# Performance work log

Hardware: AMD Instinct MI355X
Metric: run time of the kernel (lower is better)

## Reference

```python
import jax, jax.numpy as jnp
import numpy as np

N_NODES = 100000
N_EDGES = 1600000
IN_CH = 128
NHIDDEN = 64
OUT_CH = 40
NLAYERS = 4
ALPHA = 0.1


def setup_inputs() -> dict:
    key = jax.random.key(0)
    ks = jax.random.split(key, 7)
    x = jax.random.normal(ks[0], (N_NODES, IN_CH), dtype=jnp.float32)
    edge_index = jax.random.randint(ks[1], (2, N_EDGES), 0, N_NODES, dtype=jnp.int64)
    batch_graph = jnp.zeros((N_NODES,), dtype=jnp.int64)
    fc1_w = jax.random.normal(ks[2], (NHIDDEN, IN_CH), dtype=jnp.float32) * (1.0 / np.sqrt(IN_CH))
    fc1_b = jax.random.normal(ks[3], (NHIDDEN,), dtype=jnp.float32) * 0.01
    conv_w = jax.random.normal(ks[4], (NLAYERS, NHIDDEN, NHIDDEN), dtype=jnp.float32) * (1.0 / np.sqrt(NHIDDEN))
    fc2_w = jax.random.normal(ks[5], (OUT_CH, NHIDDEN), dtype=jnp.float32) * (1.0 / np.sqrt(NHIDDEN))
    fc2_b = jax.random.normal(ks[6], (OUT_CH,), dtype=jnp.float32) * 0.01
    return {"x": x, "edge_index": edge_index, "batch_graph": batch_graph,
            "fc1_w": fc1_w, "fc1_b": fc1_b, "conv_w": conv_w,
            "fc2_w": fc2_w, "fc2_b": fc2_b}


def reference(x, edge_index, batch_graph, fc1_w, fc1_b, conv_w, fc2_w, fc2_b):
    # eval mode: dropout layers are identity
    n = x.shape[0]
    row, col = edge_index[0], edge_index[1]  # source, target

    # gcn_norm with add_self_loops=False: sym deg^-1/2 normalization
    deg = jax.ops.segment_sum(jnp.ones_like(row, dtype=x.dtype), col, num_segments=n)
    dinv = jnp.where(deg > 0, deg ** -0.5, 0.0)
    norm = (dinv[row] * dinv[col])[:, None]  # [E, 1]

    h = jax.nn.relu(x @ fc1_w.T + fc1_b)  # [N, nhidden]
    h0 = h
    nlayers = conv_w.shape[0]
    for i in range(nlayers):
        # GCN2Conv: aggregate, initial-residual mix, weight1 matmul (beta=1)
        agg = jax.ops.segment_sum(h[row] * norm, col, num_segments=n)
        mixed = (1.0 - ALPHA) * agg + ALPHA * h0
        h = jax.nn.relu(mixed @ conv_w[i])
    out = h @ fc2_w.T + fc2_b  # [N, out_channels]
    return out
```

## Files before the change

### kernel.cpp

```cpp
#include <hip/hip_runtime.h>
#include <hip/hip_fp16.h>

#define N_NODES 100000
#define N_EDGES 1600000
#define IN_CH   128
#define NHID    64
#define OUT_CH  40
#define NBLK    391
#define NBUCK   196
#define BCAP    8960
#define WECAP   320
#define E4CAP   (N_EDGES + 7 * N_NODES + 64)


__global__ __launch_bounds__(256) void k_scan1(const int* __restrict__ cnt,
                                               int* __restrict__ rowptr,
                                               int* __restrict__ bsum,
                                               float* __restrict__ dinv) {
    __shared__ int s[256];
    int t = threadIdx.x;
    int n = blockIdx.x * 256 + t;
    int v = (n < N_NODES) ? cnt[n] : 0;
    int pv = (v + 7) & ~7;
    s[t] = pv;
    __syncthreads();
    for (int off = 1; off < 256; off <<= 1) {
        int add = (t >= off) ? s[t - off] : 0;
        __syncthreads();
        s[t] += add;
        __syncthreads();
    }
    int incl = s[t];
    if (n < N_NODES) {
        rowptr[n] = incl - pv;
        dinv[n] = (v > 0) ? rsqrtf((float)v) : 0.0f;
    }
    if (t == 255) bsum[blockIdx.x] = incl;
}

__global__ __launch_bounds__(512) void k_scan2(int* __restrict__ bsum,
                                               int* __restrict__ rowptr) {
    __shared__ int s[512];
    int t = threadIdx.x;
    int v = (t < NBLK) ? bsum[t] : 0;
    s[t] = v;
    __syncthreads();
    for (int off = 1; off < 512; off <<= 1) {
        int add = (t >= off) ? s[t - off] : 0;
        __syncthreads();
        s[t] += add;
        __syncthreads();
    }
    if (t == NBLK - 1) rowptr[N_NODES] = s[t];
    if (t < NBLK) bsum[t] = s[t] - v;
}

__global__ __launch_bounds__(256) void k_scan3(const int* __restrict__ bsum,
                                               int* __restrict__ rowptr) {
    int n = blockIdx.x * 256 + threadIdx.x;
    if (n < N_NODES) rowptr[n] = rowptr[n] + bsum[n >> 8];
}


__global__ __launch_bounds__(256) void k_scatA(const int* __restrict__ ei,
                                               int* __restrict__ bucketCnt,
                                               int2* __restrict__ ebufA) {
    __shared__ int hist[NBUCK];
    __shared__ int base[NBUCK];
    int t = threadIdx.x;
    int chunk = blockIdx.x * 4096;
    for (int i = t; i < NBUCK; i += 256) hist[i] = 0;
    __syncthreads();
#pragma unroll 4
    for (int i = 0; i < 16; i++) {
        int e = chunk + i * 256 + t;
        if (e < N_EDGES) atomicAdd(&hist[ei[N_EDGES + e] >> 9], 1);
    }
    __syncthreads();
    for (int b = t; b < NBUCK; b += 256) {
        int h = hist[b];
        base[b] = h ? atomicAdd(&bucketCnt[b], h) : 0;
    }
    __syncthreads();
#pragma unroll 4
    for (int i = 0; i < 16; i++) {
        int e = chunk + i * 256 + t;
        if (e < N_EDGES) {
            int r = ei[e], c = ei[N_EDGES + e];
            int pos = atomicAdd(&base[c >> 9], 1);
            ebufA[(size_t)(c >> 9) * BCAP + pos] = make_int2(r, c);
        }
    }
}


__global__ __launch_bounds__(256) void k_deg(const int2* __restrict__ ebufA,
                                             const int* __restrict__ bucketCnt,
                                             int* __restrict__ cnt) {
    __shared__ int hist[512];
    int b = blockIdx.x;
    int nodeB = b * 512;
    int t = threadIdx.x;
    for (int i = t; i < 512; i += 256) hist[i] = 0;
    __syncthreads();
    int nE = bucketCnt[b];
    const int2* src = ebufA + (size_t)b * BCAP;
    for (int i = t; i < nE; i += 256) atomicAdd(&hist[src[i].y - nodeB], 1);
    __syncthreads();
    for (int i = t; i < 512; i += 256) {
        int node = nodeB + i;
        if (node < N_NODES) cnt[node] = hist[i];
    }
}


__global__ __launch_bounds__(256) void k_scatB(const int2* __restrict__ ebufA,
                                               const int* __restrict__ bucketCnt,
                                               const int* __restrict__ rowptr,
                                               int* __restrict__ e4) {
    __shared__ int lcur[512];
    int b = blockIdx.x;
    int nodeB = b * 512;
    int t = threadIdx.x;
    for (int i = t; i < 512; i += 256) {
        int node = nodeB + i;
        lcur[i] = (node < N_NODES) ? rowptr[node] : 0;
    }
    __syncthreads();
    int nE = bucketCnt[b];
    const int2* src = ebufA + (size_t)b * BCAP;
    for (int i = t; i < nE; i += 256) {
        int2 rc = src[i];
        int pos = atomicAdd(&lcur[rc.y - nodeB], 1);
        e4[pos] = rc.x;
    }
    __syncthreads();
    for (int i = t; i < 512; i += 256) {
        int node = nodeB + i;
        if (node < N_NODES) {
            int end = rowptr[node + 1];
            for (int pos = lcur[i]; pos < end; pos++) e4[pos] = N_NODES;
        }
    }
}

__device__ __forceinline__ void store_h4(__half* dst, float a, float b, float c, float d) {
    union { uint2 u; __half2 h[2]; } pk;
    pk.h[0] = __floats2half2_rn(a, b);
    pk.h[1] = __floats2half2_rn(c, d);
    *(uint2*)dst = pk.u;
}


__global__ __launch_bounds__(256, 2) void k_fc1(const float* __restrict__ x,
                                                const float* __restrict__ w,
                                                const float* __restrict__ b,
                                                const float* __restrict__ dinv,
                                                __half* __restrict__ h016,
                                                __half* __restrict__ hs1) {
    __shared__ float xs[64 * 128];
    __shared__ float wL[64 * 128];
    int t = threadIdx.x;
    int nodeBase = blockIdx.x * 64;

    {
        int lane8 = t & 7, rhalf = t >> 3;
#pragma unroll
        for (int r2 = 0; r2 < 2; r2++) {
            int nl = r2 * 32 + rhalf;
            int swz = (nl ^ (nl >> 3)) & 7;
            int n = nodeBase + nl;
            float4* dstrow = (float4*)(xs + nl * 128);
            if (n < N_NODES) {
                const float4* src = (const float4*)(x + (size_t)n * IN_CH);
#pragma unroll
                for (int q = 0; q < 4; q++) dstrow[(q * 8 + lane8) ^ swz] = src[q * 8 + lane8];
            } else {
                float4 z = {0.f, 0.f, 0.f, 0.f};
#pragma unroll
                for (int q = 0; q < 4; q++) dstrow[(q * 8 + lane8) ^ swz] = z;
            }
            float4* dstw = (float4*)(wL + nl * 128);
            const float4* srcw = (const float4*)(w + (size_t)nl * IN_CH);
#pragma unroll
            for (int q = 0; q < 4; q++) dstw[(q * 8 + lane8) ^ swz] = srcw[q * 8 + lane8];
        }
    }
    __syncthreads();

    int tx = t & 15, ty = t >> 4;
    int o0 = tx * 4, n0 = ty * 4;
    int swzA0 = ((n0 + 0) ^ ((n0 + 0) >> 3)) & 7;
    int swzA1 = ((n0 + 1) ^ ((n0 + 1) >> 3)) & 7;
    int swzA2 = ((n0 + 2) ^ ((n0 + 2) >> 3)) & 7;
    int swzA3 = ((n0 + 3) ^ ((n0 + 3) >> 3)) & 7;
    int swzW0 = ((o0 + 0) ^ ((o0 + 0) >> 3)) & 7;
    int swzW1 = ((o0 + 1) ^ ((o0 + 1) >> 3)) & 7;
    int swzW2 = ((o0 + 2) ^ ((o0 + 2) >> 3)) & 7;
    int swzW3 = ((o0 + 3) ^ ((o0 + 3) >> 3)) & 7;
    const float4* ar0 = (const float4*)(xs + (n0 + 0) * 128);
    const float4* ar1 = (const float4*)(xs + (n0 + 1) * 128);
    const float4* ar2 = (const float4*)(xs + (n0 + 2) * 128);
    const float4* ar3 = (const float4*)(xs + (n0 + 3) * 128);
    const float4* wr0 = (const float4*)(wL + (o0 + 0) * 128);
    const float4* wr1 = (const float4*)(wL + (o0 + 1) * 128);
    const float4* wr2 = (const float4*)(wL + (o0 + 2) * 128);
    const float4* wr3 = (const float4*)(wL + (o0 + 3) * 128);

    float c[4][4];
#pragma unroll
    for (int i = 0; i < 4; i++)
#pragma unroll
        for (int j = 0; j < 4; j++) c[i][j] = 0.f;

#pragma unroll 4
    for (int k = 0; k < IN_CH; k += 4) {
        int kk = k >> 2;
        float4 b0 = wr0[kk ^ swzW0];
        float4 b1 = wr1[kk ^ swzW1];
        float4 b2 = wr2[kk ^ swzW2];
        float4 b3 = wr3[kk ^ swzW3];
        float4 a0 = ar0[kk ^ swzA0];
        float4 a1 = ar1[kk ^ swzA1];
        float4 a2 = ar2[kk ^ swzA2];
        float4 a3 = ar3[kk ^ swzA3];
#pragma unroll
        for (int i = 0; i < 4; i++) {
            float4 a = (i == 0) ? a0 : (i == 1) ? a1 : (i == 2) ? a2 : a3;
            c[i][0] = fmaf(a.x, b0.x, fmaf(a.y, b0.y, fmaf(a.z, b0.z, fmaf(a.w, b0.w, c[i][0]))));
            c[i][1] = fmaf(a.x, b1.x, fmaf(a.y, b1.y, fmaf(a.z, b1.z, fmaf(a.w, b1.w, c[i][1]))));
            c[i][2] = fmaf(a.x, b2.x, fmaf(a.y, b2.y, fmaf(a.z, b2.z, fmaf(a.w, b2.w, c[i][2]))));
            c[i][3] = fmaf(a.x, b3.x, fmaf(a.y, b3.y, fmaf(a.z, b3.z, fmaf(a.w, b3.w, c[i][3]))));
        }
    }

    float4 bias = *(const float4*)&b[o0];
#pragma unroll
    for (int i = 0; i < 4; i++) {
        int n = nodeBase + n0 + i;
        if (n < N_NODES) {
            float vx = fmaxf(c[i][0] + bias.x, 0.f);
            float vy = fmaxf(c[i][1] + bias.y, 0.f);
            float vz = fmaxf(c[i][2] + bias.z, 0.f);
            float vw = fmaxf(c[i][3] + bias.w, 0.f);
            store_h4(&h016[(size_t)n * NHID + o0], vx, vy, vz, vw);
            float dn = dinv[n];
            store_h4(&hs1[(size_t)n * NHID + o0], vx * dn, vy * dn, vz * dn, vw * dn);
        }
    }
}


__global__ __launch_bounds__(256, 4) void k_conv(const __half* __restrict__ hs,
                                                 const __half* __restrict__ h0,
                                                 const int* __restrict__ rowptr,
                                                 const int* __restrict__ e4,
                                                 const float* __restrict__ W,
                                                 const float* __restrict__ dinv,
                                                 __half* __restrict__ hout,
                                                 int scaled) {
    __shared__ int   eSw[4][WECAP];
    __shared__ float mixs[4][8 * 68];
    int t = threadIdx.x;
    int wid = t >> 6, lane = t & 63;
    int wbase = blockIdx.x * 32 + wid * 8;
    int grp = lane >> 3;
    int cg = (lane & 7) * 8;
    int* eW = eSw[wid];
    float* mix = mixs[wid];

    int n = wbase + grp;
    int s = rowptr[n], e = rowptr[n + 1];
    int wb0 = rowptr[wbase];
    int wbN = rowptr[wbase + 8] - wb0;
    int nStage = (wbN < WECAP) ? wbN : WECAP;
    for (int i = lane; i < nStage; i += 64) eW[i] = e4[wb0 + i];

#define LOADM(pm, jb)                                                    \
    {                                                                    \
        _Pragma("unroll")                                                \
        for (int u = 0; u < 4; u++) {                                    \
            int idx = (jb) + u;                                          \
            int li = idx - wb0;                                          \
            pm[u] = (li < WECAP) ? eW[li] : e4[idx];                     \
        }                                                                \
    }
#define ISSUE(pv, pm)                                                    \
    {                                                                    \
        _Pragma("unroll")                                                \
        for (int u = 0; u < 4; u++)                                      \
            pv[u] = *(const float4*)&hs[(size_t)pm[u] * NHID + cg];      \
    }
#define ACC4(cv)                                                         \
    {                                                                    \
        _Pragma("unroll")                                                \
        for (int u = 0; u < 4; u++) {                                    \
            const __half2* hp = (const __half2*)&cv[u];                  \
            _Pragma("unroll")                                            \
            for (int q = 0; q < 4; q++) {                                \
                float2 f = __half22float2(hp[q]);                        \
                acc[q * 2 + 0] += f.x;                                   \
                acc[q * 2 + 1] += f.y;                                   \
            }                                                            \
        }                                                                \
    }

    int    pmA[4], pmB[4];
    float4 pvA[4], pvB[4];
    if (e > s) {
#pragma unroll
        for (int u = 0; u < 4; u++) pmA[u] = e4[s + u];
        ISSUE(pvA, pmA);
#pragma unroll
        for (int u = 0; u < 4; u++) pmB[u] = e4[s + 4 + u];
        ISSUE(pvB, pmB);
    }

    float dn = dinv[n];
    float4 h0raw = *(const float4*)&h0[(size_t)n * NHID + cg];

    float acc[8];
#pragma unroll
    for (int i = 0; i < 8; i++) acc[i] = 0.f;

    __threadfence_block();

    for (int j = s; j < e; j += 8) {
        {
            float4 cv[4];
#pragma unroll
            for (int u = 0; u < 4; u++) cv[u] = pvA[u];
            int jn = j + 8;
            if (jn < e) { LOADM(pmA, jn); ISSUE(pvA, pmA); }
            ACC4(cv);
        }
        {
            float4 cv[4];
#pragma unroll
            for (int u = 0; u < 4; u++) cv[u] = pvB[u];
            int jn = j + 12;
            if (jn < e) { LOADM(pmB, jn); ISSUE(pvB, pmB); }
            ACC4(cv);
        }
    }
#undef LOADM
#undef ISSUE
#undef ACC4

    {
        const __half* h0h = (const __half*)&h0raw;
        float a = 0.9f * dn;
        float m[8];
#pragma unroll
        for (int q = 0; q < 8; q++)
            m[q] = fmaf(a, acc[q], 0.1f * __half2float(h0h[q]));
        float4 m0 = {m[0], m[1], m[2], m[3]};
        float4 m1 = {m[4], m[5], m[6], m[7]};
        *(float4*)&mix[grp * 68 + cg] = m0;
        *(float4*)&mix[grp * 68 + cg + 4] = m1;
    }
    __threadfence_block();

    int tx = lane & 15, ty = lane >> 4;
    int o0 = tx * 4, r0 = ty * 2;
    float c[2][4];
#pragma unroll
    for (int i = 0; i < 2; i++)
#pragma unroll
        for (int j = 0; j < 4; j++) c[i][j] = 0.f;

#pragma unroll 4
    for (int k = 0; k < NHID; k += 4) {
        float4 b0 = *(const float4*)&W[(k + 0) * NHID + o0];
        float4 b1 = *(const float4*)&W[(k + 1) * NHID + o0];
        float4 b2 = *(const float4*)&W[(k + 2) * NHID + o0];
        float4 b3 = *(const float4*)&W[(k + 3) * NHID + o0];
#pragma unroll
        for (int i = 0; i < 2; i++) {
            float4 a = *(const float4*)&mix[(r0 + i) * 68 + k];
            c[i][0] = fmaf(a.x, b0.x, fmaf(a.y, b1.x, fmaf(a.z, b2.x, fmaf(a.w, b3.x, c[i][0]))));
            c[i][1] = fmaf(a.x, b0.y, fmaf(a.y, b1.y, fmaf(a.z, b2.y, fmaf(a.w, b3.y, c[i][1]))));
            c[i][2] = fmaf(a.x, b0.z, fmaf(a.y, b1.z, fmaf(a.z, b2.z, fmaf(a.w, b3.z, c[i][2]))));
            c[i][3] = fmaf(a.x, b0.w, fmaf(a.y, b1.w, fmaf(a.z, b2.w, fmaf(a.w, b3.w, c[i][3]))));
        }
    }
#pragma unroll
    for (int i = 0; i < 2; i++) {
        int n2 = wbase + r0 + i;
        float sc = 1.0f;
        if (scaled) sc = dinv[n2];
        store_h4(&hout[(size_t)n2 * NHID + o0],
                 fmaxf(c[i][0], 0.f) * sc, fmaxf(c[i][1], 0.f) * sc,
                 fmaxf(c[i][2], 0.f) * sc, fmaxf(c[i][3], 0.f) * sc);
    }
}


__global__ __launch_bounds__(256) void k_fc2(const __half* __restrict__ h,
                                             const float* __restrict__ w,
                                             const float* __restrict__ b,
                                             float* __restrict__ out) {
    __shared__ float wT[NHID * 44];
    __shared__ float hsl[64 * 68];
    int t = threadIdx.x;
    int nodeBase = blockIdx.x * 64;

    for (int id = t; id < NHID * OUT_CH; id += 256) {
        int o = id >> 6, k = id & 63;
        wT[k * 44 + o] = w[id];
    }
    {
        int nl = t >> 2, seg = t & 3;
        int n = nodeBase + nl;
        float* dst = hsl + nl * 68 + seg * 16;
        if (n < N_NODES) {
            float4 raw0 = *(const float4*)&h[(size_t)n * NHID + seg * 16];
            float4 raw1 = *(const float4*)&h[(size_t)n * NHID + seg * 16 + 8];
            const __half2* hp0 = (const __half2*)&raw0;
            const __half2* hp1 = (const __half2*)&raw1;
#pragma unroll
            for (int q = 0; q < 4; q++) {
                float2 f = __half22float2(hp0[q]);
                dst[q * 2 + 0] = f.x;
                dst[q * 2 + 1] = f.y;
            }
#pragma unroll
            for (int q = 0; q < 4; q++) {
                float2 f = __half22float2(hp1[q]);
                dst[8 + q * 2 + 0] = f.x;
                dst[8 + q * 2 + 1] = f.y;
            }
        } else {
#pragma unroll
            for (int q = 0; q < 16; q++) dst[q] = 0.f;
        }
    }
    __syncthreads();

    if (t < 160) {
        int tx = t % 10, ty = t / 10;
        int o0 = tx * 4, n0 = ty * 4;
        float c[4][4];
#pragma unroll
        for (int i = 0; i < 4; i++)
#pragma unroll
            for (int j = 0; j < 4; j++) c[i][j] = 0.f;

#pragma unroll 4
        for (int k = 0; k < NHID; k += 4) {
            float4 b0 = *(const float4*)&wT[(k + 0) * 44 + o0];
            float4 b1 = *(const float4*)&wT[(k + 1) * 44 + o0];
            float4 b2 = *(const float4*)&wT[(k + 2) * 44 + o0];
            float4 b3 = *(const float4*)&wT[(k + 3) * 44 + o0];
#pragma unroll
            for (int i = 0; i < 4; i++) {
                float4 a = *(const float4*)&hsl[(n0 + i) * 68 + k];
                c[i][0] = fmaf(a.x, b0.x, fmaf(a.y, b1.x, fmaf(a.z, b2.x, fmaf(a.w, b3.x, c[i][0]))));
                c[i][1] = fmaf(a.x, b0.y, fmaf(a.y, b1.y, fmaf(a.z, b2.y, fmaf(a.w, b3.y, c[i][1]))));
                c[i][2] = fmaf(a.x, b0.z, fmaf(a.y, b1.z, fmaf(a.z, b2.z, fmaf(a.w, b3.z, c[i][2]))));
                c[i][3] = fmaf(a.x, b0.w, fmaf(a.y, b1.w, fmaf(a.z, b2.w, fmaf(a.w, b3.w, c[i][3]))));
            }
        }
        float4 bias = *(const float4*)&b[o0];
#pragma unroll
        for (int i = 0; i < 4; i++) {
            int n = nodeBase + n0 + i;
            if (n < N_NODES) {
                float4 v;
                v.x = c[i][0] + bias.x;
                v.y = c[i][1] + bias.y;
                v.z = c[i][2] + bias.z;
                v.w = c[i][3] + bias.w;
                *(float4*)&out[(size_t)n * OUT_CH + o0] = v;
            }
        }
    }
}


extern "C" void kernel_launch(void* const* d_in, const int* in_sizes, int n_in,
                              void* d_out, int out_size, void* d_ws, size_t ws_size,
                              hipStream_t stream) {
    const float* x    = (const float*)d_in[0];
    const int*   ei   = (const int*)d_in[1];
    const float* fc1w = (const float*)d_in[3];
    const float* fc1b = (const float*)d_in[4];
    const float* cw   = (const float*)d_in[5];
    const float* fc2w = (const float*)d_in[6];
    const float* fc2b = (const float*)d_in[7];
    float* out = (float*)d_out;

    char* p = (char*)d_ws;
    auto alloc = [&](size_t bytes) { char* r = p; p += (bytes + 255) & ~(size_t)255; return r; };
    __half* h016   = (__half*)alloc((size_t)N_NODES * NHID * 2);
    __half* hsA    = (__half*)alloc((size_t)(N_NODES + 1) * NHID * 2);
    __half* hsB    = (__half*)alloc((size_t)(N_NODES + 1) * NHID * 2);
    int*    e4     = (int*)   alloc((size_t)E4CAP * 4);
    int2*   ebufA  = (int2*)  alloc((size_t)NBUCK * BCAP * 8);
    int*    cnt    = (int*)   alloc((size_t)N_NODES * 4);
    int*    rowptr = (int*)   alloc((size_t)(N_NODES + 1) * 4);
    int*    bCnt   = (int*)   alloc((size_t)NBUCK * 4);
    float*  dinv   = (float*) alloc((size_t)N_NODES * 4);
    int*    bsum   = (int*)   alloc(512 * 4);
    __half* h4     = (__half*)ebufA;

    hipMemsetAsync(bCnt, 0, (size_t)NBUCK * 4, stream);
    hipMemsetAsync(hsA + (size_t)N_NODES * NHID, 0, NHID * 2, stream);
    hipMemsetAsync(hsB + (size_t)N_NODES * NHID, 0, NHID * 2, stream);

    k_scatA<<<(N_EDGES + 4095) / 4096, 256, 0, stream>>>(ei, bCnt, ebufA);
    k_deg  <<<NBUCK, 256, 0, stream>>>(ebufA, bCnt, cnt);
    k_scan1<<<NBLK, 256, 0, stream>>>(cnt, rowptr, bsum, dinv);
    k_scan2<<<1, 512, 0, stream>>>(bsum, rowptr);
    k_scan3<<<NBLK, 256, 0, stream>>>(bsum, rowptr);
    k_scatB<<<NBUCK, 256, 0, stream>>>(ebufA, bCnt, rowptr, e4);

    int gb64 = (N_NODES + 63) / 64;
    int gb32 = N_NODES / 32;
    k_fc1 <<<gb64, 256, 0, stream>>>(x, fc1w, fc1b, dinv, h016, hsA);
    k_conv<<<gb32, 256, 0, stream>>>(hsA, h016, rowptr, e4, cw + 0 * NHID * NHID, dinv, hsB, 1);
    k_conv<<<gb32, 256, 0, stream>>>(hsB, h016, rowptr, e4, cw + 1 * NHID * NHID, dinv, hsA, 1);
    k_conv<<<gb32, 256, 0, stream>>>(hsA, h016, rowptr, e4, cw + 2 * NHID * NHID, dinv, hsB, 1);
    k_conv<<<gb32, 256, 0, stream>>>(hsB, h016, rowptr, e4, cw + 3 * NHID * NHID, dinv, h4, 0);
    k_fc2 <<<gb64, 256, 0, stream>>>(h4, fc2w, fc2b, out);
}
```

Baseline: 409.9 us.

## Sort nodes by degree into a permutation to balance conv wavefront work

Builds a degree histogram during the degree pass, scans it, and adds a placement kernel that writes a node permutation grouped by in-degree. Conv kernels now process nodes in that order, so each wave's eight nodes have similar edge counts and less lane divergence. The LDS staging of edge indices is removed in favour of int4 vector loads from the padded CSR, and launch bounds rise to 8 blocks per CU. In exchange, nodes handled by one wave are no longer contiguous, so h0, rowptr and edge reads lose locality, and one extra kernel is added to preprocessing.

Result: slower. 941.5 us (+129.7%).

```diff
diff --git a/kernel.cpp b/kernel.cpp
--- a/kernel.cpp
+++ b/kernel.cpp
@@ -9,7 +9,6 @@
 #define NBLK    391
 #define NBUCK   196
 #define BCAP    8960
-#define WECAP   320
 #define E4CAP   (N_EDGES + 7 * N_NODES + 64)
 
 
@@ -39,11 +38,15 @@
 }
 
 __global__ __launch_bounds__(512) void k_scan2(int* __restrict__ bsum,
-                                               int* __restrict__ rowptr) {
+                                               int* __restrict__ rowptr,
+                                               const int* __restrict__ gbins,
+                                               int* __restrict__ binCur) {
     __shared__ int s[512];
+    __shared__ int sb[64];
     int t = threadIdx.x;
     int v = (t < NBLK) ? bsum[t] : 0;
     s[t] = v;
+    if (t < 64) sb[t] = gbins[t];
     __syncthreads();
     for (int off = 1; off < 512; off <<= 1) {
         int add = (t >= off) ? s[t - off] : 0;
@@ -53,12 +56,48 @@
     }
     if (t == NBLK - 1) rowptr[N_NODES] = s[t];
     if (t < NBLK) bsum[t] = s[t] - v;
+    for (int off = 1; off < 64; off <<= 1) {
+        int add = (t >= off && t < 64) ? sb[t - off] : 0;
+        __syncthreads();
+        if (t < 64) sb[t] += add;
+        __syncthreads();
+    }
+    if (t < 64) binCur[t] = sb[t] - gbins[t];
 }
 
 __global__ __launch_bounds__(256) void k_scan3(const int* __restrict__ bsum,
                                                int* __restrict__ rowptr) {
     int n = blockIdx.x * 256 + threadIdx.x;
     if (n < N_NODES) rowptr[n] = rowptr[n] + bsum[n >> 8];
+}
+
+
+__global__ __launch_bounds__(256) void k_place(const int* __restrict__ cnt,
+                                               int* __restrict__ binCur,
+                                               int* __restrict__ perm) {
+    __shared__ int hist[64];
+    __shared__ int base[64];
+    int t = threadIdx.x;
+    int n = blockIdx.x * 256 + t;
+    if (t < 64) hist[t] = 0;
+    __syncthreads();
+    int bin = -1;
+    if (n < N_NODES) {
+        int d = cnt[n];
+        bin = (d < 63) ? d : 63;
+        atomicAdd(&hist[bin], 1);
+    }
+    __syncthreads();
+    if (t < 64) {
+        int h = hist[t];
+        base[t] = h ? atomicAdd(&binCur[t], h) : 0;
+        hist[t] = 0;
+    }
+    __syncthreads();
+    if (n < N_NODES) {
+        int off = atomicAdd(&hist[bin], 1);
+        perm[base[bin] + off] = n;
+    }
 }
 
 
@@ -96,12 +135,15 @@
 
 __global__ __launch_bounds__(256) void k_deg(const int2* __restrict__ ebufA,
                                              const int* __restrict__ bucketCnt,
-                                             int* __restrict__ cnt) {
+                                             int* __restrict__ cnt,
+                                             int* __restrict__ gbins) {
     __shared__ int hist[512];
+    __shared__ int dbins[64];
     int b = blockIdx.x;
     int nodeB = b * 512;
     int t = threadIdx.x;
     for (int i = t; i < 512; i += 256) hist[i] = 0;
+    if (t < 64) dbins[t] = 0;
     __syncthreads();
     int nE = bucketCnt[b];
     const int2* src = ebufA + (size_t)b * BCAP;
@@ -109,8 +151,14 @@
     __syncthreads();
     for (int i = t; i < 512; i += 256) {
         int node = nodeB + i;
-        if (node < N_NODES) cnt[node] = hist[i];
-    }
+        if (node < N_NODES) {
+            int h = hist[i];
+            cnt[node] = h;
+            atomicAdd(&dbins[(h < 63) ? h : 63], 1);
+        }
+    }
+    __syncthreads();
+    if (t < 64 && dbins[t]) atomicAdd(&gbins[t], dbins[t]);
 }
 
 
@@ -251,45 +299,32 @@
 }
 
 
-__global__ __launch_bounds__(256, 4) void k_conv(const __half* __restrict__ hs,
+__global__ __launch_bounds__(256, 8) void k_conv(const __half* __restrict__ hs,
                                                  const __half* __restrict__ h0,
                                                  const int* __restrict__ rowptr,
                                                  const int* __restrict__ e4,
                                                  const float* __restrict__ W,
                                                  const float* __restrict__ dinv,
+                                                 const int* __restrict__ perm,
                                                  __half* __restrict__ hout,
                                                  int scaled) {
-    __shared__ int   eSw[4][WECAP];
     __shared__ float mixs[4][8 * 68];
     int t = threadIdx.x;
     int wid = t >> 6, lane = t & 63;
-    int wbase = blockIdx.x * 32 + wid * 8;
+    int wslot = blockIdx.x * 32 + wid * 8;
     int grp = lane >> 3;
     int cg = (lane & 7) * 8;
-    int* eW = eSw[wid];
     float* mix = mixs[wid];
 
-    int n = wbase + grp;
+    int n = perm[wslot + grp];
     int s = rowptr[n], e = rowptr[n + 1];
-    int wb0 = rowptr[wbase];
-    int wbN = rowptr[wbase + 8] - wb0;
-    int nStage = (wbN < WECAP) ? wbN : WECAP;
-    for (int i = lane; i < nStage; i += 64) eW[i] = e4[wb0 + i];
-
-#define LOADM(pm, jb)                                                    \
-    {                                                                    \
-        _Pragma("unroll")                                                \
-        for (int u = 0; u < 4; u++) {                                    \
-            int idx = (jb) + u;                                          \
-            int li = idx - wb0;                                          \
-            pm[u] = (li < WECAP) ? eW[li] : e4[idx];                     \
-        }                                                                \
-    }
+
 #define ISSUE(pv, pm)                                                    \
     {                                                                    \
-        _Pragma("unroll")                                                \
-        for (int u = 0; u < 4; u++)                                      \
-            pv[u] = *(const float4*)&hs[(size_t)pm[u] * NHID + cg];      \
+        pv[0] = *(const float4*)&hs[(size_t)pm.x * NHID + cg];           \
+        pv[1] = *(const float4*)&hs[(size_t)pm.y * NHID + cg];           \
+        pv[2] = *(const float4*)&hs[(size_t)pm.z * NHID + cg];           \
+        pv[3] = *(const float4*)&hs[(size_t)pm.w * NHID + cg];           \
     }
 #define ACC4(cv)                                                         \
     {                                                                    \
@@ -305,14 +340,12 @@
         }                                                                \
     }
 
-    int    pmA[4], pmB[4];
+    int4   pmA, pmB;
     float4 pvA[4], pvB[4];
     if (e > s) {
-#pragma unroll
-        for (int u = 0; u < 4; u++) pmA[u] = e4[s + u];
+        pmA = *(const int4*)&e4[s];
         ISSUE(pvA, pmA);
-#pragma unroll
-        for (int u = 0; u < 4; u++) pmB[u] = e4[s + 4 + u];
+        pmB = *(const int4*)&e4[s + 4];
         ISSUE(pvB, pmB);
     }
 
@@ -322,8 +355,6 @@
     float acc[8];
 #pragma unroll
     for (int i = 0; i < 8; i++) acc[i] = 0.f;
-
-    __threadfence_block();
 
     for (int j = s; j < e; j += 8) {
         {
@@ -331,7 +362,7 @@
 #pragma unroll
             for (int u = 0; u < 4; u++) cv[u] = pvA[u];
             int jn = j + 8;
-            if (jn < e) { LOADM(pmA, jn); ISSUE(pvA, pmA); }
+            if (jn < e) { pmA = *(const int4*)&e4[jn]; ISSUE(pvA, pmA); }
             ACC4(cv);
         }
         {
@@ -339,11 +370,10 @@
 #pragma unroll
             for (int u = 0; u < 4; u++) cv[u] = pvB[u];
             int jn = j + 12;
-            if (jn < e) { LOADM(pmB, jn); ISSUE(pvB, pmB); }
+            if (jn < e) { pmB = *(const int4*)&e4[jn]; ISSUE(pvB, pmB); }
             ACC4(cv);
         }
     }
-#undef LOADM
 #undef ISSUE
 #undef ACC4
 
@@ -386,7 +416,7 @@
     }
 #pragma unroll
     for (int i = 0; i < 2; i++) {
-        int n2 = wbase + r0 + i;
+        int n2 = perm[wslot + r0 + i];
         float sc = 1.0f;
         if (scaled) sc = dinv[n2];
         store_h4(&hout[(size_t)n2 * NHID + o0],
@@ -499,28 +529,33 @@
     int2*   ebufA  = (int2*)  alloc((size_t)NBUCK * BCAP * 8);
     int*    cnt    = (int*)   alloc((size_t)N_NODES * 4);
     int*    rowptr = (int*)   alloc((size_t)(N_NODES + 1) * 4);
+    int*    perm   = (int*)   alloc((size_t)N_NODES * 4);
     int*    bCnt   = (int*)   alloc((size_t)NBUCK * 4);
     float*  dinv   = (float*) alloc((size_t)N_NODES * 4);
     int*    bsum   = (int*)   alloc(512 * 4);
+    int*    gbins  = (int*)   alloc(64 * 4);
+    int*    binCur = (int*)   alloc(64 * 4);
     __half* h4     = (__half*)ebufA;
 
     hipMemsetAsync(bCnt, 0, (size_t)NBUCK * 4, stream);
+    hipMemsetAsync(gbins, 0, 64 * 4, stream);
     hipMemsetAsync(hsA + (size_t)N_NODES * NHID, 0, NHID * 2, stream);
     hipMemsetAsync(hsB + (size_t)N_NODES * NHID, 0, NHID * 2, stream);
 
     k_scatA<<<(N_EDGES + 4095) / 4096, 256, 0, stream>>>(ei, bCnt, ebufA);
-    k_deg  <<<NBUCK, 256, 0, stream>>>(ebufA, bCnt, cnt);
+    k_deg  <<<NBUCK, 256, 0, stream>>>(ebufA, bCnt, cnt, gbins);
     k_scan1<<<NBLK, 256, 0, stream>>>(cnt, rowptr, bsum, dinv);
-    k_scan2<<<1, 512, 0, stream>>>(bsum, rowptr);
+    k_scan2<<<1, 512, 0, stream>>>(bsum, rowptr, gbins, binCur);
     k_scan3<<<NBLK, 256, 0, stream>>>(bsum, rowptr);
+    k_place<<<NBLK, 256, 0, stream>>>(cnt, binCur, perm);
     k_scatB<<<NBUCK, 256, 0, stream>>>(ebufA, bCnt, rowptr, e4);
 
     int gb64 = (N_NODES + 63) / 64;
     int gb32 = N_NODES / 32;
     k_fc1 <<<gb64, 256, 0, stream>>>(x, fc1w, fc1b, dinv, h016, hsA);
-    k_conv<<<gb32, 256, 0, stream>>>(hsA, h016, rowptr, e4, cw + 0 * NHID * NHID, dinv, hsB, 1);
-    k_conv<<<gb32, 256, 0, stream>>>(hsB, h016, rowptr, e4, cw + 1 * NHID * NHID, dinv, hsA, 1);
-    k_conv<<<gb32, 256, 0, stream>>>(hsA, h016, rowptr, e4, cw + 2 * NHID * NHID, dinv, hsB, 1);
-    k_conv<<<gb32, 256, 0, stream>>>(hsB, h016, rowptr, e4, cw + 3 * NHID * NHID, dinv, h4, 0);
+    k_conv<<<gb32, 256, 0, stream>>>(hsA, h016, rowptr, e4, cw + 0 * NHID * NHID, dinv, perm, hsB, 1);
+    k_conv<<<gb32, 256, 0, stream>>>(hsB, h016, rowptr, e4, cw + 1 * NHID * NHID, dinv, perm, hsA, 1);
+    k_conv<<<gb32, 256, 0, stream>>>(hsA, h016, rowptr, e4, cw + 2 * NHID * NHID, dinv, perm, hsB, 1);
+    k_conv<<<gb32, 256, 0, stream>>>(hsB, h016, rowptr, e4, cw + 3 * NHID * NHID, dinv, perm, h4, 0);
     k_fc2 <<<gb64, 256, 0, stream>>>(h4, fc2w, fc2b, out);
 }
```
